# Kernel optimization log

Measured on AMD Instinct MI355X. Metric: run time of the kernel, lower is better.

The kernel has to match this reference:

```python
import jax, jax.numpy as jnp
import numpy as np

H = 16  # head_num

def _rope(x, cos, sin):
    # x: [B,H,T,dh]; cos/sin: [T, dh//2]
    xr = x.reshape(*x.shape[:-1], -1, 2)
    re, im = xr[..., 0], xr[..., 1]
    out_re = re * cos - im * sin
    out_im = re * sin + im * cos
    return jnp.stack([out_re, out_im], axis=-1).reshape(x.shape)

def setup_inputs() -> dict:
    key = jax.random.key(0)
    ks = jax.random.split(key, 5)
    B, T, D = 2, 2048, 1024
    s = 1.0 / np.sqrt(D)
    return {
        "embedding_word": jax.random.normal(ks[0], (B, T, D), jnp.float32),
        "wq": jax.random.normal(ks[1], (D, D), jnp.float32) * s,
        "wk": jax.random.normal(ks[2], (D, D), jnp.float32) * s,
        "wv": jax.random.normal(ks[3], (D, D), jnp.float32) * s,
        "wo": jax.random.normal(ks[4], (D, D), jnp.float32) * s,
    }

def reference(embedding_word, wq, wk, wv, wo):
    x = embedding_word
    B, T, D = x.shape
    dh = D // H
    # projections (torch Linear: x @ W.T)
    q = (x @ wq.T).reshape(B, T, H, dh).transpose(0, 2, 1, 3)  # [B,H,T,dh]
    k = (x @ wk.T).reshape(B, T, H, dh).transpose(0, 2, 1, 3)
    v = (x @ wv.T).reshape(B, T, H, dh).transpose(0, 2, 1, 3)
    # rotary embedding (theta=10000)
    freqs = 1.0 / (10000.0 ** (jnp.arange(0, dh, 2, dtype=jnp.float32) / dh))
    ang = jnp.arange(T, dtype=jnp.float32)[:, None] * freqs[None, :]  # [T, dh/2]
    cos, sin = jnp.cos(ang), jnp.sin(ang)
    q = _rope(q, cos, sin)
    k = _rope(k, cos, sin)
    # attention with causal mask; scale after mask as in original
    scores = jnp.einsum("bhqd,bhkd->bhqk", q, k)
    causal = jnp.triu(jnp.ones((T, T), dtype=bool), k=1)
    scores = jnp.where(causal, -jnp.inf, scores)
    weights = jax.nn.softmax(scores / jnp.sqrt(jnp.float32(dh)), axis=-1)
    out = jnp.einsum("bhqk,bhkd->bhqd", weights, v)
    out = out.transpose(0, 2, 1, 3).reshape(B, T, D)
    return out @ wo.T
```

## Files before the change

kernel.cpp:

```cpp
#include <hip/hip_runtime.h>
#include <hip/hip_bf16.h>
#include <math.h>

#define B_  2
#define T_  2048
#define D_  1024
#define H_  16
#define DH_ 64
#define TOK (B_*T_)

typedef __attribute__((ext_vector_type(8)))  short bf16x8;
typedef __attribute__((ext_vector_type(4)))  float f32x4;
typedef __attribute__((ext_vector_type(16))) float f32x16;

static __device__ __forceinline__ float bf2f(short u) {
    union { unsigned int i; float f; } c;
    c.i = ((unsigned int)(unsigned short)u) << 16;
    return c.f;
}
static __device__ __forceinline__ short f2bf(float f) {
    union { float f; unsigned int i; } c; c.f = f;
    unsigned int r = c.i + 0x7fff + ((c.i >> 16) & 1);
    return (short)(r >> 16);
}
static __device__ __forceinline__ unsigned cvtpk(float lo, float hi2) {
    unsigned r;
    asm("v_cvt_pk_bf16_f32 %0, %1, %2" : "=v"(r) : "v"(lo), "v"(hi2));
    return r;
}

__global__ __launch_bounds__(256) void cast_all(
    const float* __restrict__ x,  const float* __restrict__ wq,
    const float* __restrict__ wk, const float* __restrict__ wv,
    const float* __restrict__ wo,
    short* __restrict__ xb,  short* __restrict__ wqb,
    short* __restrict__ wkb, short* __restrict__ wvb,
    short* __restrict__ wob)
{
    int i = blockIdx.x * 256 + threadIdx.x;
    const float* src; short* dst; int off;
    if (i < 524288) { src = x; dst = xb; off = i; }
    else {
        int j = i - 524288;
        int wsel = j >> 17;  off = j & 131071;
        src = wsel == 0 ? wq : wsel == 1 ? wk : wsel == 2 ? wv : wo;
        dst = wsel == 0 ? wqb : wsel == 1 ? wkb : wsel == 2 ? wvb : wob;
    }
    const float4* p = reinterpret_cast<const float4*>(src);
    float4 a = p[2*off], b = p[2*off+1];
    bf16x8 o;
    o[0] = f2bf(a.x); o[1] = f2bf(a.y); o[2] = f2bf(a.z); o[3] = f2bf(a.w);
    o[4] = f2bf(b.x); o[5] = f2bf(b.y); o[6] = f2bf(b.z); o[7] = f2bf(b.w);
    reinterpret_cast<bf16x8*>(dst)[off] = o;
}

__global__ __launch_bounds__(256) void rope_table(float2* __restrict__ tab)
{
    int idx = blockIdx.x * 256 + threadIdx.x;
    int t = idx >> 5, i = idx & 31;
    float freq = __powf(10000.f, -(float)i * (1.0f / 32.0f));
    float s, c;
    sincosf((float)t * freq, &s, &c);
    tab[idx] = make_float2(c, s);
}

__global__ __launch_bounds__(256) void rope_apply2(short* __restrict__ Q,
                                                   short* __restrict__ K,
                                                   const float2* __restrict__ tab)
{
    int g = blockIdx.x * 256 + threadIdx.x;
    short* X;
    float sc;
    int q;
    if (g < 524288) { X = Q; sc = 0.18033688011112042f; q = g; }
    else            { X = K; sc = 1.0f;                 q = g - 524288; }
    int p0 = q << 2;
    int tt = (p0 >> 9) & (T_ - 1);
    int i0 = p0 & 31;
    int4 v = reinterpret_cast<int4*>(X)[q];
    int out[4]; int vv[4] = {v.x, v.y, v.z, v.w};
#pragma unroll
    for (int j = 0; j < 4; ++j) {
        float2 cs = tab[tt * 32 + i0 + j];
        float re = bf2f((short)(vv[j] & 0xffff));
        float im = bf2f((short)(((unsigned int)vv[j]) >> 16));
        float nr = (re * cs.x - im * cs.y) * sc;
        float ni = (re * cs.y + im * cs.x) * sc;
        out[j] = (int)(unsigned short)f2bf(nr) |
                 ((int)(unsigned short)f2bf(ni) << 16);
    }
    reinterpret_cast<int4*>(X)[q] = make_int4(out[0], out[1], out[2], out[3]);
}

template<int BF16OUT>
__global__ __launch_bounds__(256) void gemm_abt_mfma(
    const short* __restrict__ A,
    const short* __restrict__ B0, const short* __restrict__ B1, const short* __restrict__ B2,
    short* __restrict__ Ob0, short* __restrict__ Ob1, short* __restrict__ Ob2,
    float* __restrict__ Of0, int K)
{
    __shared__ short As[128 * 32];
    __shared__ short Bs[128 * 32];
    const int sel = blockIdx.x >> 3;
    const int bn  = (blockIdx.x & 7) << 7;
    const int bm  = blockIdx.y << 7;
    const short* Bm = sel == 0 ? B0 : (sel == 1 ? B1 : B2);
    short* Obp      = sel == 0 ? Ob0 : (sel == 1 ? Ob1 : Ob2);
    const int tid  = threadIdx.x;
    const int wv   = tid >> 6, lane = tid & 63;
    const int wr   = wv >> 1,  wc   = wv & 1;
    const int fr   = lane & 15, fg  = lane >> 4;
    const int srow  = lane >> 2;
    const int skoff = (lane & 3) << 3;
    f32x4 acc[4][4] = {};

    for (int k0 = 0; k0 < K; k0 += 32) {
        __syncthreads();
#pragma unroll
        for (int it = 0; it < 2; ++it) {
            const int c = wv * 2 + it;
            const int r = 16 * c + srow;
            __builtin_amdgcn_global_load_lds(
                (const __attribute__((address_space(1))) unsigned int*)
                    (A + (size_t)(bm + r) * K + k0 + skoff),
                (__attribute__((address_space(3))) unsigned int*)(As + c * 512),
                16, 0, 0);
            __builtin_amdgcn_global_load_lds(
                (const __attribute__((address_space(1))) unsigned int*)
                    (Bm + (size_t)(bn + r) * K + k0 + skoff),
                (__attribute__((address_space(3))) unsigned int*)(Bs + c * 512),
                16, 0, 0);
        }
        __syncthreads();
        bf16x8 af[4], bfr[4];
#pragma unroll
        for (int m = 0; m < 4; ++m)
            af[m] = *(const bf16x8*)(As + (wr * 64 + m * 16 + fr) * 32 + fg * 8);
#pragma unroll
        for (int n = 0; n < 4; ++n)
            bfr[n] = *(const bf16x8*)(Bs + (wc * 64 + n * 16 + fr) * 32 + fg * 8);
#pragma unroll
        for (int m = 0; m < 4; ++m)
#pragma unroll
            for (int n = 0; n < 4; ++n)
                acc[m][n] = __builtin_amdgcn_mfma_f32_16x16x32_bf16(
                                af[m], bfr[n], acc[m][n], 0, 0, 0);
    }
    const int row0 = bm + wr * 64 + fg * 4;
    const int col0 = bn + wc * 64 + fr;
#pragma unroll
    for (int m = 0; m < 4; ++m)
#pragma unroll
        for (int n = 0; n < 4; ++n)
#pragma unroll
            for (int j = 0; j < 4; ++j) {
                const size_t idx = (size_t)(row0 + m * 16 + j) * 1024 + col0 + n * 16;
                if (BF16OUT) Obp[idx] = f2bf(acc[m][n][j]);
                else         Of0[idx] = acc[m][n][j];
            }
}

__global__ __launch_bounds__(256) void attn_mfma2(
    const short* __restrict__ Qb, const short* __restrict__ Kb,
    const short* __restrict__ Vb, short* __restrict__ Ob)
{
    __shared__ short KsBuf[2][64 * 64];
    __shared__ short VtBuf[2][64 * 64];

    const int qb = (int)(gridDim.x - 1 - blockIdx.x);
    const int bh = blockIdx.y;
    const int b  = bh >> 4, h = bh & 15;
    const int q0 = qb << 7;
    const int tid  = threadIdx.x;
    const int w    = tid >> 6, lane = tid & 63;
    const int ql   = lane & 31, hi = lane >> 5;
    const int qw_lo  = q0 + 32 * w;
    const int q_glob = qw_lo + ql;
    const int nt = (q0 + 128) >> 6;

    const short* qp = Qb + (size_t)(b * T_ + q_glob) * D_ + h * DH_ + hi * 8;
    bf16x8 qf[4];
#pragma unroll
    for (int ds = 0; ds < 4; ++ds)
        qf[ds] = *(const bf16x8*)(qp + 16 * ds);

    float m_run = -3e38f, l_run = 0.f;
    f32x16 accO0, accO1;
#pragma unroll
    for (int r = 0; r < 16; ++r) { accO0[r] = 0.f; accO1[r] = 0.f; }

    const int sr0 = tid >> 3, sr1 = sr0 + 32, sdo = (tid & 7) << 3;
    const short* kbase = Kb + (size_t)b * T_ * D_ + h * DH_ + sdo;
    const short* vbase = Vb + (size_t)b * T_ * D_ + h * DH_ + sdo;

    bf16x8 krA, krB, vrA, vrB;
#define LOADT(t) {                                                        \
        const size_t o_ = (size_t)((t) << 6) * D_;                        \
        krA = *(const bf16x8*)(kbase + o_ + (size_t)sr0 * D_);            \
        krB = *(const bf16x8*)(kbase + o_ + (size_t)sr1 * D_);            \
        vrA = *(const bf16x8*)(vbase + o_ + (size_t)sr0 * D_);            \
        vrB = *(const bf16x8*)(vbase + o_ + (size_t)sr1 * D_); }
#define STORET(bu) {                                                      \
        short* Kp = KsBuf[bu]; short* Vp = VtBuf[bu];                     \
        *(bf16x8*)(Kp + ((sr0 * 64 + sdo) ^ ((sr0 & 7) << 3))) = krA;     \
        *(bf16x8*)(Kp + ((sr1 * 64 + sdo) ^ ((sr1 & 7) << 3))) = krB;     \
        _Pragma("unroll")                                                 \
        for (int jj = 0; jj < 8; ++jj) {                                  \
            const int j0 = (jj + (tid & 7)) & 7;                          \
            const int d0 = sdo + j0;                                      \
            Vp[(d0 * 64 + sr0) ^ ((d0 & 7) << 3)] = vrA[j0];              \
            Vp[(d0 * 64 + sr1) ^ ((d0 & 7) << 3)] = vrB[j0];              \
        } }

    LOADT(0); STORET(0);
    __syncthreads();

    for (int t = 0; t < nt; ++t) {
        const int cur = t & 1;
        const int K0  = t << 6;
        const bool hasNext = (t + 1 < nt);
        if (hasNext) LOADT(t + 1);

        if (K0 <= qw_lo + 31) {
            const short* Kp = KsBuf[cur];
            const short* Vp = VtBuf[cur];
            f32x16 s0, s1;
#pragma unroll
            for (int r = 0; r < 16; ++r) { s0[r] = 0.f; s1[r] = 0.f; }
#pragma unroll
            for (int ds = 0; ds < 4; ++ds) {
                const int c = 16 * ds + 8 * hi;
                const int r0 = ql, r1 = 32 + ql;
                bf16x8 kf0 = *(const bf16x8*)(Kp + ((r0 * 64 + c) ^ ((r0 & 7) << 3)));
                bf16x8 kf1 = *(const bf16x8*)(Kp + ((r1 * 64 + c) ^ ((r1 & 7) << 3)));
                s0 = __builtin_amdgcn_mfma_f32_32x32x16_bf16(kf0, qf[ds], s0, 0, 0, 0);
                s1 = __builtin_amdgcn_mfma_f32_32x32x16_bf16(kf1, qf[ds], s1, 0, 0, 0);
            }
            if (K0 + 63 > qw_lo) {
                const int qrel = q_glob - K0;
#pragma unroll
                for (int r = 0; r < 16; ++r) {
                    const int kv0 = 4 * hi + ((r & 3) + 8 * (r >> 2));
                    s0[r] = (kv0      <= qrel) ? s0[r] : -3e38f;
                    s1[r] = (kv0 + 32 <= qrel) ? s1[r] : -3e38f;
                }
            }
            float mloc = s0[0];
#pragma unroll
            for (int r = 1; r < 16; ++r) mloc = fmaxf(mloc, s0[r]);
#pragma unroll
            for (int r = 0; r < 16; ++r) mloc = fmaxf(mloc, s1[r]);
            mloc = fmaxf(mloc, __shfl_xor(mloc, 32));
            if (!__all(mloc <= m_run + 11.5f)) {
                const float mnew = fmaxf(m_run, mloc);
                const float corr = exp2f(m_run - mnew);
                m_run = mnew;
                l_run *= corr;
#pragma unroll
                for (int r = 0; r < 16; ++r) { accO0[r] *= corr; accO1[r] *= corr; }
            }
            float lsum = 0.f;
#pragma unroll
            for (int r = 0; r < 16; ++r) { s0[r] = exp2f(s0[r] - m_run); lsum += s0[r]; }
#pragma unroll
            for (int r = 0; r < 16; ++r) { s1[r] = exp2f(s1[r] - m_run); lsum += s1[r]; }
            lsum += __shfl_xor(lsum, 32);
            l_run += lsum;
            unsigned W[8][2];
#pragma unroll
            for (int q4 = 0; q4 < 4; ++q4) {
                W[q4][0]     = cvtpk(s0[4*q4+0], s0[4*q4+1]);
                W[q4][1]     = cvtpk(s0[4*q4+2], s0[4*q4+3]);
                W[q4 + 4][0] = cvtpk(s1[4*q4+0], s1[4*q4+1]);
                W[q4 + 4][1] = cvtpk(s1[4*q4+2], s1[4*q4+3]);
            }
#pragma unroll
            for (int sl = 0; sl < 4; ++sl) {
                const int qe = 2 * sl, qo = qe + 1;
                unsigned srcA = hi ? W[qe][0] : W[qo][0];
                unsigned srcB = hi ? W[qe][1] : W[qo][1];
                unsigned xA = (unsigned)__shfl_xor((int)srcA, 32);
                unsigned xB = (unsigned)__shfl_xor((int)srcB, 32);
                union { unsigned u[4]; bf16x8 v; } pu;
                pu.u[0] = hi ? xA : W[qe][0];
                pu.u[1] = hi ? xB : W[qe][1];
                pu.u[2] = hi ? W[qo][0] : xA;
                pu.u[3] = hi ? W[qo][1] : xB;
                const int c = 16 * sl + 8 * hi;
                const int d0 = ql, d1 = 32 + ql;
                bf16x8 vf0 = *(const bf16x8*)(Vp + ((d0 * 64 + c) ^ ((d0 & 7) << 3)));
                bf16x8 vf1 = *(const bf16x8*)(Vp + ((d1 * 64 + c) ^ ((d1 & 7) << 3)));
                accO0 = __builtin_amdgcn_mfma_f32_32x32x16_bf16(vf0, pu.v, accO0, 0, 0, 0);
                accO1 = __builtin_amdgcn_mfma_f32_32x32x16_bf16(vf1, pu.v, accO1, 0, 0, 0);
            }
        }
        if (hasNext) STORET(cur ^ 1);
        __syncthreads();
    }

    unsigned* Ot = (unsigned*)KsBuf;
    const float invl = 1.f / l_run;
#pragma unroll
    for (int rq = 0; rq < 4; ++rq) {
        unsigned p0 = cvtpk(accO0[4*rq+0] * invl, accO0[4*rq+1] * invl);
        unsigned p1 = cvtpk(accO0[4*rq+2] * invl, accO0[4*rq+3] * invl);
        unsigned p2 = cvtpk(accO1[4*rq+0] * invl, accO1[4*rq+1] * invl);
        unsigned p3 = cvtpk(accO1[4*rq+2] * invl, accO1[4*rq+3] * invl);
        const int du0 = (4 * hi + 8 * rq) >> 1;
        Ot[w * 1024 + ql * 32 + du0]          = p0;
        Ot[w * 1024 + ql * 32 + du0 + 1]      = p1;
        Ot[w * 1024 + ql * 32 + du0 + 16]     = p2;
        Ot[w * 1024 + ql * 32 + du0 + 16 + 1] = p3;
    }
    __syncthreads();
    {
        const int qq = tid >> 1, half = tid & 1;
        const int4* s4 = (const int4*)(Ot + (qq >> 5) * 1024 + (qq & 31) * 32 + half * 16);
        int4* d4 = (int4*)(Ob + (size_t)(b * T_ + q0 + qq) * D_ + h * DH_ + half * 32);
        d4[0] = s4[0]; d4[1] = s4[1]; d4[2] = s4[2]; d4[3] = s4[3];
    }
#undef LOADT
#undef STORET
}

extern "C" void kernel_launch(void* const* d_in, const int* in_sizes, int n_in,
                              void* d_out, int out_size, void* d_ws, size_t ws_size,
                              hipStream_t stream)
{
    const float* x  = (const float*)d_in[0];
    const float* wq = (const float*)d_in[1];
    const float* wk = (const float*)d_in[2];
    const float* wv = (const float*)d_in[3];
    const float* wo = (const float*)d_in[4];
    float* out = (float*)d_out;

    const size_t NTOK = (size_t)TOK * D_;
    const size_t NW   = (size_t)D_ * D_;
    short* xb  = (short*)d_ws;
    short* wqb = xb  + NTOK;
    short* wkb = wqb + NW;
    short* wvb = wkb + NW;
    short* wob = wvb + NW;
    short* Qb  = wob + NW;
    short* Kb  = Qb  + NTOK;
    short* Vb  = Kb  + NTOK;
    short* Obf = Vb  + NTOK;
    float2* tab = (float2*)(Obf + NTOK);

    cast_all<<<4096, 256, 0, stream>>>(x, wq, wk, wv, wo,
                                       xb, wqb, wkb, wvb, wob);
    rope_table<<<256, 256, 0, stream>>>(tab);

    gemm_abt_mfma<1><<<dim3(24, 32), 256, 0, stream>>>(
        xb, wqb, wkb, wvb, Qb, Kb, Vb, nullptr, D_);

    rope_apply2<<<4096, 256, 0, stream>>>(Qb, Kb, tab);

    attn_mfma2<<<dim3(T_ / 128, B_ * H_), 256, 0, stream>>>(Qb, Kb, Vb, Obf);

    gemm_abt_mfma<0><<<dim3(8, 32), 256, 0, stream>>>(
        Obf, wob, wob, wob, nullptr, nullptr, nullptr, out, D_);
}
```

Baseline: 276.7 us.

## Write V transposed from QKV GEMM and load attention operands directly from global

The QKV GEMM now writes V in a transposed [b,h,d,t] layout through an LDS staging tile, so the attention kernel can read V fragments straight from global memory without an in-kernel transpose. The attention kernel drops its LDS double buffering and syncs: each wave loads its own K/V fragments from global, skips the upper 32-key half on diagonal tiles, and uses a remapped 1D grid ordering. The rope table generation is merged into the cast kernel to save a launch. The risks are more redundant global/L2 traffic per wave and a GEMM epilogue that needs an extra 34 KB of LDS.

```diff
diff --git a/kernel.cpp b/kernel.cpp
--- a/kernel.cpp
+++ b/kernel.cpp
@@ -6,7 +6,6 @@
 #define T_  2048
 #define D_  1024
 #define H_  16
-#define DH_ 64
 #define TOK (B_*T_)
 
 typedef __attribute__((ext_vector_type(8)))  short bf16x8;
@@ -29,15 +28,25 @@
     return r;
 }
 
-__global__ __launch_bounds__(256) void cast_all(
+__global__ __launch_bounds__(256) void cast_table(
     const float* __restrict__ x,  const float* __restrict__ wq,
     const float* __restrict__ wk, const float* __restrict__ wv,
     const float* __restrict__ wo,
     short* __restrict__ xb,  short* __restrict__ wqb,
     short* __restrict__ wkb, short* __restrict__ wvb,
-    short* __restrict__ wob)
-{
-    int i = blockIdx.x * 256 + threadIdx.x;
+    short* __restrict__ wob, float2* __restrict__ tab)
+{
+    const int bid = blockIdx.x;
+    if (bid >= 4096) {
+        int idx = (bid - 4096) * 256 + threadIdx.x;
+        int t = idx >> 5, i = idx & 31;
+        float freq = __powf(10000.f, -(float)i * (1.0f / 32.0f));
+        float s, c;
+        sincosf((float)t * freq, &s, &c);
+        tab[idx] = make_float2(c, s);
+        return;
+    }
+    int i = bid * 256 + threadIdx.x;
     const float* src; short* dst; int off;
     if (i < 524288) { src = x; dst = xb; off = i; }
     else {
@@ -52,16 +61,6 @@
     o[0] = f2bf(a.x); o[1] = f2bf(a.y); o[2] = f2bf(a.z); o[3] = f2bf(a.w);
     o[4] = f2bf(b.x); o[5] = f2bf(b.y); o[6] = f2bf(b.z); o[7] = f2bf(b.w);
     reinterpret_cast<bf16x8*>(dst)[off] = o;
-}
-
-__global__ __launch_bounds__(256) void rope_table(float2* __restrict__ tab)
-{
-    int idx = blockIdx.x * 256 + threadIdx.x;
-    int t = idx >> 5, i = idx & 31;
-    float freq = __powf(10000.f, -(float)i * (1.0f / 32.0f));
-    float s, c;
-    sincosf((float)t * freq, &s, &c);
-    tab[idx] = make_float2(c, s);
 }
 
 __global__ __launch_bounds__(256) void rope_apply2(short* __restrict__ Q,
@@ -101,6 +100,7 @@
 {
     __shared__ short As[128 * 32];
     __shared__ short Bs[128 * 32];
+    __shared__ short Tb[128 * 136];
     const int sel = blockIdx.x >> 3;
     const int bn  = (blockIdx.x & 7) << 7;
     const int bm  = blockIdx.y << 7;
@@ -146,6 +146,33 @@
                 acc[m][n] = __builtin_amdgcn_mfma_f32_16x16x32_bf16(
                                 af[m], bfr[n], acc[m][n], 0, 0, 0);
     }
+
+    if (BF16OUT && sel == 2) {
+#pragma unroll
+        for (int m = 0; m < 4; ++m)
+#pragma unroll
+            for (int n = 0; n < 4; ++n) {
+                const int dl = wc * 64 + n * 16 + fr;
+                const int tk = wr * 64 + m * 16 + fg * 4;
+                unsigned lo  = cvtpk(acc[m][n][0], acc[m][n][1]);
+                unsigned hi2 = cvtpk(acc[m][n][2], acc[m][n][3]);
+                *(unsigned*)(Tb + dl * 136 + tk)     = lo;
+                *(unsigned*)(Tb + dl * 136 + tk + 2) = hi2;
+            }
+        __syncthreads();
+        const int bb = bm >> 11;
+#pragma unroll
+        for (int it = 0; it < 8; ++it) {
+            const int c  = it * 256 + tid;
+            const int dl = c >> 4;
+            const int off = (c & 15) << 3;
+            bf16x8 v = *(const bf16x8*)(Tb + dl * 136 + off);
+            *(bf16x8*)(Obp + (size_t)(bb * 1024 + bn + dl) * 2048
+                             + (bm & 2047) + off) = v;
+        }
+        return;
+    }
+
     const int row0 = bm + wr * 64 + fg * 4;
     const int col0 = bn + wc * 64 + fr;
 #pragma unroll
@@ -160,25 +187,25 @@
             }
 }
 
-__global__ __launch_bounds__(256) void attn_mfma2(
+__global__ __launch_bounds__(256) void attn_v3(
     const short* __restrict__ Qb, const short* __restrict__ Kb,
-    const short* __restrict__ Vb, short* __restrict__ Ob)
-{
-    __shared__ short KsBuf[2][64 * 64];
-    __shared__ short VtBuf[2][64 * 64];
-
-    const int qb = (int)(gridDim.x - 1 - blockIdx.x);
-    const int bh = blockIdx.y;
+    const short* __restrict__ Vt, short* __restrict__ Ob)
+{
+    __shared__ unsigned Ot[4 * 1152];
+
+    const int tid = threadIdx.x;
+    const int w = tid >> 6, lane = tid & 63;
+    const int ql = lane & 31, hi = lane >> 5;
+    const int dd = (int)blockIdx.x;
+    const int L  = (dd & 7) * 64 + (dd >> 3);
+    const int bh = L >> 4;
+    const int qb = 15 - (L & 15);
     const int b  = bh >> 4, h = bh & 15;
-    const int q0 = qb << 7;
-    const int tid  = threadIdx.x;
-    const int w    = tid >> 6, lane = tid & 63;
-    const int ql   = lane & 31, hi = lane >> 5;
-    const int qw_lo  = q0 + 32 * w;
-    const int q_glob = qw_lo + ql;
-    const int nt = (q0 + 128) >> 6;
-
-    const short* qp = Qb + (size_t)(b * T_ + q_glob) * D_ + h * DH_ + hi * 8;
+    const int q0 = qb * 128 + w * 32;
+    const int q_glob = q0 + ql;
+    const int nt = (q0 >> 6) + 1;
+
+    const short* qp = Qb + (size_t)(b * T_ + q_glob) * D_ + h * 64 + hi * 8;
     bf16x8 qf[4];
 #pragma unroll
     for (int ds = 0; ds < 4; ++ds)
@@ -189,93 +216,96 @@
 #pragma unroll
     for (int r = 0; r < 16; ++r) { accO0[r] = 0.f; accO1[r] = 0.f; }
 
-    const int sr0 = tid >> 3, sr1 = sr0 + 32, sdo = (tid & 7) << 3;
-    const short* kbase = Kb + (size_t)b * T_ * D_ + h * DH_ + sdo;
-    const short* vbase = Vb + (size_t)b * T_ * D_ + h * DH_ + sdo;
-
-    bf16x8 krA, krB, vrA, vrB;
-#define LOADT(t) {                                                        \
-        const size_t o_ = (size_t)((t) << 6) * D_;                        \
-        krA = *(const bf16x8*)(kbase + o_ + (size_t)sr0 * D_);            \
-        krB = *(const bf16x8*)(kbase + o_ + (size_t)sr1 * D_);            \
-        vrA = *(const bf16x8*)(vbase + o_ + (size_t)sr0 * D_);            \
-        vrB = *(const bf16x8*)(vbase + o_ + (size_t)sr1 * D_); }
-#define STORET(bu) {                                                      \
-        short* Kp = KsBuf[bu]; short* Vp = VtBuf[bu];                     \
-        *(bf16x8*)(Kp + ((sr0 * 64 + sdo) ^ ((sr0 & 7) << 3))) = krA;     \
-        *(bf16x8*)(Kp + ((sr1 * 64 + sdo) ^ ((sr1 & 7) << 3))) = krB;     \
-        _Pragma("unroll")                                                 \
-        for (int jj = 0; jj < 8; ++jj) {                                  \
-            const int j0 = (jj + (tid & 7)) & 7;                          \
-            const int d0 = sdo + j0;                                      \
-            Vp[(d0 * 64 + sr0) ^ ((d0 & 7) << 3)] = vrA[j0];              \
-            Vp[(d0 * 64 + sr1) ^ ((d0 & 7) << 3)] = vrB[j0];              \
-        } }
-
-    LOADT(0); STORET(0);
-    __syncthreads();
+    const short* kbase = Kb + (size_t)(b * T_) * D_ + h * 64 + hi * 8;
+    const short* vbase = Vt + (size_t)(bh * 64) * 2048 + hi * 8;
 
     for (int t = 0; t < nt; ++t) {
-        const int cur = t & 1;
-        const int K0  = t << 6;
-        const bool hasNext = (t + 1 < nt);
-        if (hasNext) LOADT(t + 1);
-
-        if (K0 <= qw_lo + 31) {
-            const short* Kp = KsBuf[cur];
-            const short* Vp = VtBuf[cur];
-            f32x16 s0, s1;
-#pragma unroll
-            for (int r = 0; r < 16; ++r) { s0[r] = 0.f; s1[r] = 0.f; }
-#pragma unroll
-            for (int ds = 0; ds < 4; ++ds) {
-                const int c = 16 * ds + 8 * hi;
-                const int r0 = ql, r1 = 32 + ql;
-                bf16x8 kf0 = *(const bf16x8*)(Kp + ((r0 * 64 + c) ^ ((r0 & 7) << 3)));
-                bf16x8 kf1 = *(const bf16x8*)(Kp + ((r1 * 64 + c) ^ ((r1 & 7) << 3)));
-                s0 = __builtin_amdgcn_mfma_f32_32x32x16_bf16(kf0, qf[ds], s0, 0, 0, 0);
-                s1 = __builtin_amdgcn_mfma_f32_32x32x16_bf16(kf1, qf[ds], s1, 0, 0, 0);
-            }
-            if (K0 + 63 > qw_lo) {
-                const int qrel = q_glob - K0;
+        const int K0 = t << 6;
+        const bool diag  = (K0 + 63 > q0);
+        const bool useHi = (K0 + 32 <= q0 + 31);
+
+        const short* kp = kbase + (size_t)K0 * D_;
+        bf16x8 kf0[4], kf1[4];
+#pragma unroll
+        for (int ds = 0; ds < 4; ++ds)
+            kf0[ds] = *(const bf16x8*)(kp + (size_t)ql * D_ + 16 * ds);
+        if (useHi) {
+#pragma unroll
+            for (int ds = 0; ds < 4; ++ds)
+                kf1[ds] = *(const bf16x8*)(kp + (size_t)(32 + ql) * D_ + 16 * ds);
+        }
+
+        f32x16 s0, s1;
+#pragma unroll
+        for (int r = 0; r < 16; ++r) { s0[r] = 0.f; s1[r] = 0.f; }
+#pragma unroll
+        for (int ds = 0; ds < 4; ++ds)
+            s0 = __builtin_amdgcn_mfma_f32_32x32x16_bf16(kf0[ds], qf[ds], s0, 0, 0, 0);
+        if (useHi) {
+#pragma unroll
+            for (int ds = 0; ds < 4; ++ds)
+                s1 = __builtin_amdgcn_mfma_f32_32x32x16_bf16(kf1[ds], qf[ds], s1, 0, 0, 0);
+        }
+
+        if (diag) {
+            const int qrel = q_glob - K0;
+#pragma unroll
+            for (int r = 0; r < 16; ++r) {
+                const int kv0 = 4 * hi + (r & 3) + 8 * (r >> 2);
+                s0[r] = (kv0 <= qrel) ? s0[r] : -3e38f;
+            }
+            if (useHi) {
 #pragma unroll
                 for (int r = 0; r < 16; ++r) {
-                    const int kv0 = 4 * hi + ((r & 3) + 8 * (r >> 2));
-                    s0[r] = (kv0      <= qrel) ? s0[r] : -3e38f;
+                    const int kv0 = 4 * hi + (r & 3) + 8 * (r >> 2);
                     s1[r] = (kv0 + 32 <= qrel) ? s1[r] : -3e38f;
                 }
             }
-            float mloc = s0[0];
-#pragma unroll
-            for (int r = 1; r < 16; ++r) mloc = fmaxf(mloc, s0[r]);
+        }
+
+        float mloc = s0[0];
+#pragma unroll
+        for (int r = 1; r < 16; ++r) mloc = fmaxf(mloc, s0[r]);
+        if (useHi) {
 #pragma unroll
             for (int r = 0; r < 16; ++r) mloc = fmaxf(mloc, s1[r]);
-            mloc = fmaxf(mloc, __shfl_xor(mloc, 32));
-            if (!__all(mloc <= m_run + 11.5f)) {
-                const float mnew = fmaxf(m_run, mloc);
-                const float corr = exp2f(m_run - mnew);
-                m_run = mnew;
-                l_run *= corr;
-#pragma unroll
-                for (int r = 0; r < 16; ++r) { accO0[r] *= corr; accO1[r] *= corr; }
-            }
-            float lsum = 0.f;
-#pragma unroll
-            for (int r = 0; r < 16; ++r) { s0[r] = exp2f(s0[r] - m_run); lsum += s0[r]; }
+        }
+        mloc = fmaxf(mloc, __shfl_xor(mloc, 32));
+        if (!__all(mloc <= m_run + 11.5f)) {
+            const float mnew = fmaxf(m_run, mloc);
+            const float corr = exp2f(m_run - mnew);
+            m_run = mnew;
+            l_run *= corr;
+#pragma unroll
+            for (int r = 0; r < 16; ++r) { accO0[r] *= corr; accO1[r] *= corr; }
+        }
+        float lsum = 0.f;
+#pragma unroll
+        for (int r = 0; r < 16; ++r) { s0[r] = exp2f(s0[r] - m_run); lsum += s0[r]; }
+        if (useHi) {
 #pragma unroll
             for (int r = 0; r < 16; ++r) { s1[r] = exp2f(s1[r] - m_run); lsum += s1[r]; }
-            lsum += __shfl_xor(lsum, 32);
-            l_run += lsum;
-            unsigned W[8][2];
+        }
+        lsum += __shfl_xor(lsum, 32);
+        l_run += lsum;
+
+        unsigned W[8][2];
+#pragma unroll
+        for (int q4 = 0; q4 < 4; ++q4) {
+            W[q4][0] = cvtpk(s0[4*q4+0], s0[4*q4+1]);
+            W[q4][1] = cvtpk(s0[4*q4+2], s0[4*q4+3]);
+        }
+        if (useHi) {
 #pragma unroll
             for (int q4 = 0; q4 < 4; ++q4) {
-                W[q4][0]     = cvtpk(s0[4*q4+0], s0[4*q4+1]);
-                W[q4][1]     = cvtpk(s0[4*q4+2], s0[4*q4+3]);
                 W[q4 + 4][0] = cvtpk(s1[4*q4+0], s1[4*q4+1]);
                 W[q4 + 4][1] = cvtpk(s1[4*q4+2], s1[4*q4+3]);
             }
-#pragma unroll
-            for (int sl = 0; sl < 4; ++sl) {
+        }
+
+#pragma unroll
+        for (int sl = 0; sl < 4; ++sl) {
+            if (sl < 2 || useHi) {
                 const int qe = 2 * sl, qo = qe + 1;
                 unsigned srcA = hi ? W[qe][0] : W[qo][0];
                 unsigned srcB = hi ? W[qe][1] : W[qo][1];
@@ -286,19 +316,14 @@
                 pu.u[1] = hi ? xB : W[qe][1];
                 pu.u[2] = hi ? W[qo][0] : xA;
                 pu.u[3] = hi ? W[qo][1] : xB;
-                const int c = 16 * sl + 8 * hi;
-                const int d0 = ql, d1 = 32 + ql;
-                bf16x8 vf0 = *(const bf16x8*)(Vp + ((d0 * 64 + c) ^ ((d0 & 7) << 3)));
-                bf16x8 vf1 = *(const bf16x8*)(Vp + ((d1 * 64 + c) ^ ((d1 & 7) << 3)));
+                bf16x8 vf0 = *(const bf16x8*)(vbase + (size_t)ql * 2048        + K0 + 16 * sl);
+                bf16x8 vf1 = *(const bf16x8*)(vbase + (size_t)(32 + ql) * 2048 + K0 + 16 * sl);
                 accO0 = __builtin_amdgcn_mfma_f32_32x32x16_bf16(vf0, pu.v, accO0, 0, 0, 0);
                 accO1 = __builtin_amdgcn_mfma_f32_32x32x16_bf16(vf1, pu.v, accO1, 0, 0, 0);
             }
         }
-        if (hasNext) STORET(cur ^ 1);
-        __syncthreads();
-    }
-
-    unsigned* Ot = (unsigned*)KsBuf;
+    }
+
     const float invl = 1.f / l_run;
 #pragma unroll
     for (int rq = 0; rq < 4; ++rq) {
@@ -306,21 +331,19 @@
         unsigned p1 = cvtpk(accO0[4*rq+2] * invl, accO0[4*rq+3] * invl);
         unsigned p2 = cvtpk(accO1[4*rq+0] * invl, accO1[4*rq+1] * invl);
         unsigned p3 = cvtpk(accO1[4*rq+2] * invl, accO1[4*rq+3] * invl);
-        const int du0 = (4 * hi + 8 * rq) >> 1;
-        Ot[w * 1024 + ql * 32 + du0]          = p0;
-        Ot[w * 1024 + ql * 32 + du0 + 1]      = p1;
-        Ot[w * 1024 + ql * 32 + du0 + 16]     = p2;
-        Ot[w * 1024 + ql * 32 + du0 + 16 + 1] = p3;
+        const int du0 = 4 * rq + 2 * hi;
+        Ot[w * 1152 + ql * 36 + du0]      = p0;
+        Ot[w * 1152 + ql * 36 + du0 + 1]  = p1;
+        Ot[w * 1152 + ql * 36 + du0 + 16] = p2;
+        Ot[w * 1152 + ql * 36 + du0 + 17] = p3;
     }
     __syncthreads();
     {
         const int qq = tid >> 1, half = tid & 1;
-        const int4* s4 = (const int4*)(Ot + (qq >> 5) * 1024 + (qq & 31) * 32 + half * 16);
-        int4* d4 = (int4*)(Ob + (size_t)(b * T_ + q0 + qq) * D_ + h * DH_ + half * 32);
+        const int4* s4 = (const int4*)(Ot + (qq >> 5) * 1152 + (qq & 31) * 36 + half * 16);
+        int4* d4 = (int4*)(Ob + (size_t)(b * T_ + qb * 128 + qq) * D_ + h * 64 + half * 32);
         d4[0] = s4[0]; d4[1] = s4[1]; d4[2] = s4[2]; d4[3] = s4[3];
     }
-#undef LOADT
-#undef STORET
 }
 
 extern "C" void kernel_launch(void* const* d_in, const int* in_sizes, int n_in,
@@ -343,20 +366,19 @@
     short* wob = wvb + NW;
     short* Qb  = wob + NW;
     short* Kb  = Qb  + NTOK;
-    short* Vb  = Kb  + NTOK;
-    short* Obf = Vb  + NTOK;
+    short* Vtr = Kb  + NTOK;
+    short* Obf = Vtr + NTOK;
     float2* tab = (float2*)(Obf + NTOK);
 
-    cast_all<<<4096, 256, 0, stream>>>(x, wq, wk, wv, wo,
-                                       xb, wqb, wkb, wvb, wob);
-    rope_table<<<256, 256, 0, stream>>>(tab);
+    cast_table<<<4352, 256, 0, stream>>>(x, wq, wk, wv, wo,
+                                         xb, wqb, wkb, wvb, wob, tab);
 
     gemm_abt_mfma<1><<<dim3(24, 32), 256, 0, stream>>>(
-        xb, wqb, wkb, wvb, Qb, Kb, Vb, nullptr, D_);
+        xb, wqb, wkb, wvb, Qb, Kb, Vtr, nullptr, D_);
 
     rope_apply2<<<4096, 256, 0, stream>>>(Qb, Kb, tab);
 
-    attn_mfma2<<<dim3(T_ / 128, B_ * H_), 256, 0, stream>>>(Qb, Kb, Vb, Obf);
+    attn_v3<<<512, 256, 0, stream>>>(Qb, Kb, Vtr, Obf);
 
     gemm_abt_mfma<0><<<dim3(8, 32), 256, 0, stream>>>(
         Obf, wob, wob, wob, nullptr, nullptr, nullptr, out, D_);
```

After: 280.1 us. Within noise of the previous version (+1.2%).
